# Performance work log

Measured on AMD Instinct MI355X. Metric: run time of the kernel, lower is better.

The kernel has to match this reference:

```python
import jax, jax.numpy as jnp
import numpy as np

HID = 256
NH = 8
HD = HID // NH
B = 4096
N = 64


def _xavier(key, shape):
    fan_in, fan_out = shape
    lim = float(np.sqrt(6.0 / (fan_in + fan_out)))
    return jax.random.uniform(key, shape, jnp.float32, -lim, lim)


def setup_inputs() -> dict:
    key = jax.random.key(0)
    ks = jax.random.split(key, 16)
    inp = {
        "h_recv": jax.random.normal(ks[0], (B, HID), jnp.float32),
        "h_send": jax.random.normal(ks[1], (B, N, HID), jnp.float32),
        "dist_matrix": jax.random.uniform(ks[2], (B, N), jnp.float32),
        "mask": jax.random.randint(ks[3], (B, N), 0, 2, jnp.int32),
        # projection weights stored as [in, out] (transposed vs torch Linear)
        "wq_w": _xavier(ks[4], (HID, HID)), "wq_b": jnp.zeros((HID,), jnp.float32),
        "wk_w": _xavier(ks[5], (HID, HID)), "wk_b": jnp.zeros((HID,), jnp.float32),
        "wv_w": _xavier(ks[6], (HID, HID)), "wv_b": jnp.zeros((HID,), jnp.float32),
        "d1_w": _xavier(ks[7], (HID, HID // 2)), "d1_b": jnp.zeros((HID // 2,), jnp.float32),
        "d2_w": _xavier(ks[8], (HID // 2, NH)), "d2_b": jnp.zeros((NH,), jnp.float32),
    }
    return inp


def reference(h_recv, h_send, dist_matrix, mask,
              wq_w, wq_b, wk_w, wk_b, wv_w, wv_b,
              d1_w, d1_b, d2_w, d2_b):
    b, n, hid = h_send.shape
    nh = d2_b.shape[0]
    hd = hid // nh
    # projections
    Q = (h_recv @ wq_w + wq_b).reshape(b, nh, hd)            # [B,H,D]
    K = (h_send @ wk_w + wk_b).reshape(b, n, nh, hd)          # [B,N,H,D]
    V = (h_send @ wv_w + wv_b).reshape(b, n, nh, hd)          # [B,N,H,D]
    # single-query scores per head
    scores = jnp.einsum('bhd,bnhd->bnh', Q, K) / (hd ** 0.5)  # [B,N,H]
    # MLP distance bias (softplus ensures positive slope)
    b1 = jax.nn.softplus(jax.nn.relu(h_recv @ d1_w + d1_b) @ d2_w + d2_b)  # [B,H]
    scores = scores - b1[:, None, :] * dist_matrix[:, :, None]
    # mask: zero entries -> -inf
    scores = jnp.where(mask[:, :, None] != 0, scores, -jnp.inf)
    attn = jax.nn.softmax(scores, axis=1)                     # softmax over neighbors
    z = jnp.einsum('bnh,bnhd->bhd', attn, V).reshape(b, hid)  # [B,hidden]
    return z, attn
```

## Files before the change

kernel.cpp:

```cpp
#include <hip/hip_runtime.h>
#include <math.h>

#define B_   4096
#define N_   64
#define HID_ 256
#define NH_  8
#define HD_  32
#define INV_SQRT_HD 0.17677669529663687f

typedef const float __attribute__((address_space(1)))* gbl_fp;
typedef float __attribute__((address_space(3)))* lds_fp;

__global__ __launch_bounds__(256, 2) void k1_proj(
    const float* __restrict__ h_recv,
    const float* __restrict__ wq_w, const float* __restrict__ wq_b,
    const float* __restrict__ wk_w, const float* __restrict__ wk_b,
    const float* __restrict__ d1_w, const float* __restrict__ d1_b,
    const float* __restrict__ d2_w, const float* __restrict__ d2_b,
    float* __restrict__ qh_ws, float* __restrict__ b1_ws, float* __restrict__ konst_ws)
{
    __shared__ __align__(16) float hr[8][256];
    __shared__ __align__(16) float Q[8][256];
    __shared__ float R1[8][128];
    const int t = threadIdx.x;
    const int brow = blockIdx.x * 8;

    {
        const float4* src = (const float4*)(h_recv + (size_t)brow * 256);
        float4* dst = (float4*)&hr[0][0];
        dst[t] = src[t];
        dst[t + 256] = src[t + 256];
    }
    __syncthreads();

    {
        const int j = t;
        float acc[8];
        const float bq = wq_b[j];
#pragma unroll
        for (int bb = 0; bb < 8; bb++) acc[bb] = bq;
        for (int c4 = 0; c4 < 64; c4++) {
            const float w0 = wq_w[(c4 * 4 + 0) * 256 + j];
            const float w1 = wq_w[(c4 * 4 + 1) * 256 + j];
            const float w2 = wq_w[(c4 * 4 + 2) * 256 + j];
            const float w3 = wq_w[(c4 * 4 + 3) * 256 + j];
#pragma unroll
            for (int bb = 0; bb < 8; bb++) {
                const float4 h = *(const float4*)&hr[bb][c4 * 4];
                acc[bb] += h.x * w0 + h.y * w1 + h.z * w2 + h.w * w3;
            }
        }
#pragma unroll
        for (int bb = 0; bb < 8; bb++) Q[bb][j] = acc[bb];
    }
    __syncthreads();

    {
        const int j = t & 127;
        const int bg = t >> 7;
        float acc[4];
        const float bd = d1_b[j];
#pragma unroll
        for (int r = 0; r < 4; r++) acc[r] = bd;
        for (int c4 = 0; c4 < 64; c4++) {
            const float w0 = d1_w[(c4 * 4 + 0) * 128 + j];
            const float w1 = d1_w[(c4 * 4 + 1) * 128 + j];
            const float w2 = d1_w[(c4 * 4 + 2) * 128 + j];
            const float w3 = d1_w[(c4 * 4 + 3) * 128 + j];
#pragma unroll
            for (int r = 0; r < 4; r++) {
                const float4 h = *(const float4*)&hr[bg * 4 + r][c4 * 4];
                acc[r] += h.x * w0 + h.y * w1 + h.z * w2 + h.w * w3;
            }
        }
#pragma unroll
        for (int r = 0; r < 4; r++) R1[bg * 4 + r][j] = fmaxf(acc[r], 0.0f);
    }
    __syncthreads();

    if (t < 64) {
        const int bb = t >> 3, h = t & 7;
        float acc = d2_b[h];
        for (int jj = 0; jj < 128; jj++) acc += R1[bb][jj] * d2_w[jj * 8 + h];
        const float sp = (acc > 20.0f) ? acc : log1pf(expf(acc));
        b1_ws[(size_t)(brow + bb) * 8 + h] = sp;
        float k = 0.0f;
        for (int d = 0; d < 32; d++) k += Q[bb][h * 32 + d] * wk_b[h * 32 + d];
        konst_ws[(size_t)(brow + bb) * 8 + h] = k * INV_SQRT_HD;
    }

    {
        const int c = t;
        for (int h = 0; h < 8; h++) {
            float acc[8] = {0, 0, 0, 0, 0, 0, 0, 0};
#pragma unroll
            for (int d4 = 0; d4 < 8; d4++) {
                const float4 w = *(const float4*)&wk_w[(size_t)c * 256 + h * 32 + d4 * 4];
#pragma unroll
                for (int bb = 0; bb < 8; bb++) {
                    const float4 q = *(const float4*)&Q[bb][h * 32 + d4 * 4];
                    acc[bb] += q.x * w.x + q.y * w.y + q.z * w.z + q.w * w.w;
                }
            }
#pragma unroll
            for (int bb = 0; bb < 8; bb++)
                qh_ws[((size_t)(brow + bb) * 8 + h) * 256 + c] = acc[bb];
        }
    }
}

__global__ __launch_bounds__(256, 2) void k2_attn(
    const float* __restrict__ h_send,
    const float* __restrict__ dist, const int* __restrict__ mask,
    const float* __restrict__ qh_ws, const float* __restrict__ b1_ws,
    const float* __restrict__ konst_ws,
    const float* __restrict__ wv_w, const float* __restrict__ wv_b,
    float* __restrict__ z_out,
    float* __restrict__ attn_out)
{
    __shared__ __align__(16) float hs[64][260];
    __shared__ __align__(16) float qh2[8][4][68];
    __shared__ __align__(16) float sc4[64][8];
    __shared__ float dist_l[64];
    __shared__ float b1_l[8], kon_l[8];
    __shared__ int mask_l[64];

    const int t = threadIdx.x;
    const int b = blockIdx.x;
    const int w = t >> 6;
    const int l = t & 63;

    {
        const float* src = h_send + (size_t)b * 16384;
#pragma unroll
        for (int i = 0; i < 16; i++) {
            const int row = i * 4 + w;
            __builtin_amdgcn_global_load_lds((gbl_fp)(src + row * 256 + l * 4),
                                             (lds_fp)&hs[row][0], 16, 0, 0);
        }
    }
    {
        const float4* qsrc = (const float4*)(qh_ws + (size_t)b * 2048);
#pragma unroll
        for (int k = 0; k < 2; k++) {
            const int e = t + k * 256;
            const float4 v = qsrc[e];
            const int h = e >> 6;
            const int qq = (e & 63) >> 4;
            const int pos = (e & 15) * 4;
            *(float4*)&qh2[h][qq][pos] = v;
        }
        if (t < 64) {
            dist_l[t] = dist[(size_t)b * 64 + t];
            mask_l[t] = mask[(size_t)b * 64 + t];
        } else if (t < 72) {
            b1_l[t - 64] = b1_ws[(size_t)b * 8 + (t - 64)];
            kon_l[t - 64] = konst_ws[(size_t)b * 8 + (t - 64)];
        }
    }
    __syncthreads();

    {
        const int n = w * 16 + (l & 15);
        const int cq = l >> 4;
        float p[8] = {0, 0, 0, 0, 0, 0, 0, 0};
#pragma unroll 4
        for (int c4 = 0; c4 < 16; c4++) {
            const float4 hv = *(const float4*)&hs[n][cq * 64 + c4 * 4];
#pragma unroll
            for (int h = 0; h < 8; h++) {
                const float4 qv = *(const float4*)&qh2[h][cq][c4 * 4];
                p[h] += hv.x * qv.x + hv.y * qv.y + hv.z * qv.z + hv.w * qv.w;
            }
        }
#pragma unroll
        for (int h = 0; h < 8; h++) {
            p[h] += __shfl_xor(p[h], 16, 64);
            p[h] += __shfl_xor(p[h], 32, 64);
        }
        if (cq == 0) {
            const float dv = dist_l[n];
            const int mv = mask_l[n];
#pragma unroll
            for (int h = 0; h < 8; h++) {
                const float s = p[h] * INV_SQRT_HD + kon_l[h] - b1_l[h] * dv;
                sc4[n][h] = mv ? s : -1e30f;
            }
        }
    }
    __syncthreads();

    {
        const int h = 2 * w + (l >> 5);
        const int n0 = l & 31;
        const float v0 = sc4[n0][h], v1 = sc4[n0 + 32][h];
        float m = fmaxf(v0, v1);
#pragma unroll
        for (int s = 1; s < 32; s <<= 1) m = fmaxf(m, __shfl_xor(m, s, 64));
        const float e0 = __expf(v0 - m), e1 = __expf(v1 - m);
        float sum = e0 + e1;
#pragma unroll
        for (int s = 1; s < 32; s <<= 1) sum += __shfl_xor(sum, s, 64);
        const float inv = 1.0f / sum;
        sc4[n0][h] = e0 * inv;
        sc4[n0 + 32][h] = e1 * inv;
    }
    __syncthreads();

    {
        const float* sl = &sc4[0][0];
        attn_out[(size_t)b * 512 + t] = sl[t];
        attn_out[(size_t)b * 512 + t + 256] = sl[t + 256];
    }

    float acc[8] = {0, 0, 0, 0, 0, 0, 0, 0};
    {
        const int c = t;
        for (int n = 0; n < 64; n += 2) {
            const float4 a0 = *(const float4*)&sc4[n][0];
            const float4 a1 = *(const float4*)&sc4[n][4];
            const float4 c0 = *(const float4*)&sc4[n + 1][0];
            const float4 c1 = *(const float4*)&sc4[n + 1][4];
            const float h0 = hs[n][c];
            const float h1 = hs[n + 1][c];
            acc[0] += a0.x * h0 + c0.x * h1;
            acc[1] += a0.y * h0 + c0.y * h1;
            acc[2] += a0.z * h0 + c0.z * h1;
            acc[3] += a0.w * h0 + c0.w * h1;
            acc[4] += a1.x * h0 + c1.x * h1;
            acc[5] += a1.y * h0 + c1.y * h1;
            acc[6] += a1.z * h0 + c1.z * h1;
            acc[7] += a1.w * h0 + c1.w * h1;
        }
    }
    {
        float* cl = &qh2[0][0][0];
#pragma unroll
        for (int h = 0; h < 8; h++) cl[h * 272 + t] = acc[h];
    }
    __syncthreads();

    {
        const int j = t;
        const float* cl = &qh2[0][0][0] + (j >> 5) * 272;
        float accz = wv_b[j];
        for (int c4 = 0; c4 < 64; c4++) {
            const float4 cv = *(const float4*)&cl[c4 * 4];
            accz += cv.x * wv_w[(c4 * 4 + 0) * 256 + j]
                  + cv.y * wv_w[(c4 * 4 + 1) * 256 + j]
                  + cv.z * wv_w[(c4 * 4 + 2) * 256 + j]
                  + cv.w * wv_w[(c4 * 4 + 3) * 256 + j];
        }
        z_out[(size_t)b * 256 + j] = accz;
    }
}

extern "C" void kernel_launch(void* const* d_in, const int* in_sizes, int n_in,
                              void* d_out, int out_size, void* d_ws, size_t ws_size,
                              hipStream_t stream)
{
    const float* h_recv = (const float*)d_in[0];
    const float* h_send = (const float*)d_in[1];
    const float* dist   = (const float*)d_in[2];
    const int*   mask   = (const int*)d_in[3];
    const float* wq_w = (const float*)d_in[4];
    const float* wq_b = (const float*)d_in[5];
    const float* wk_w = (const float*)d_in[6];
    const float* wk_b = (const float*)d_in[7];
    const float* wv_w = (const float*)d_in[8];
    const float* wv_b = (const float*)d_in[9];
    const float* d1_w = (const float*)d_in[10];
    const float* d1_b = (const float*)d_in[11];
    const float* d2_w = (const float*)d_in[12];
    const float* d2_b = (const float*)d_in[13];

    float* z_out = (float*)d_out;
    float* attn_out = (float*)d_out + (size_t)B_ * HID_;

    float* ws = (float*)d_ws;
    const size_t QH = (size_t)B_ * 8 * 256;
    float* qh_ws = ws;
    float* b1_ws = ws + QH;
    float* konst_ws = b1_ws + (size_t)B_ * 8;

    k1_proj<<<512, 256, 0, stream>>>(h_recv, wq_w, wq_b, wk_w, wk_b,
                                     d1_w, d1_b, d2_w, d2_b,
                                     qh_ws, b1_ws, konst_ws);
    k2_attn<<<B_, 256, 0, stream>>>(h_send, dist, mask, qh_ws, b1_ws, konst_ws,
                                    wv_w, wv_b, z_out, attn_out);
}
```

Measured before the change: 514.8 us.

## Drop LDS staging of h_send in attention kernel and halve rows per projection block

The attention kernel no longer copies each batch's 64x256 h_send tile into shared memory. It reads it straight from global memory twice, once row-wise for the scores and once column-wise for the weighted sum, and relies on L2/cache for the second pass. This frees about 66KB of LDS per block so more blocks fit per CU (launch bounds raised to 6). The projection kernel now processes 4 rows per block instead of 8 with twice as many blocks, adds unroll pragmas, and reads the weights twice as often in exchange for more parallelism.

```diff
diff --git a/kernel.cpp b/kernel.cpp
--- a/kernel.cpp
+++ b/kernel.cpp
@@ -8,10 +8,7 @@
 #define HD_  32
 #define INV_SQRT_HD 0.17677669529663687f
 
-typedef const float __attribute__((address_space(1)))* gbl_fp;
-typedef float __attribute__((address_space(3)))* lds_fp;
-
-__global__ __launch_bounds__(256, 2) void k1_proj(
+__global__ __launch_bounds__(256, 4) void k1_proj(
     const float* __restrict__ h_recv,
     const float* __restrict__ wq_w, const float* __restrict__ wq_b,
     const float* __restrict__ wk_w, const float* __restrict__ wk_b,
@@ -19,66 +16,67 @@
     const float* __restrict__ d2_w, const float* __restrict__ d2_b,
     float* __restrict__ qh_ws, float* __restrict__ b1_ws, float* __restrict__ konst_ws)
 {
-    __shared__ __align__(16) float hr[8][256];
-    __shared__ __align__(16) float Q[8][256];
-    __shared__ float R1[8][128];
+    __shared__ __align__(16) float hr[4][256];
+    __shared__ __align__(16) float Q[4][256];
+    __shared__ float R1[4][128];
     const int t = threadIdx.x;
-    const int brow = blockIdx.x * 8;
+    const int brow = blockIdx.x * 4;
 
     {
         const float4* src = (const float4*)(h_recv + (size_t)brow * 256);
         float4* dst = (float4*)&hr[0][0];
         dst[t] = src[t];
-        dst[t + 256] = src[t + 256];
     }
     __syncthreads();
 
     {
         const int j = t;
-        float acc[8];
+        float acc[4];
         const float bq = wq_b[j];
 #pragma unroll
-        for (int bb = 0; bb < 8; bb++) acc[bb] = bq;
+        for (int r = 0; r < 4; r++) acc[r] = bq;
+#pragma unroll 4
         for (int c4 = 0; c4 < 64; c4++) {
             const float w0 = wq_w[(c4 * 4 + 0) * 256 + j];
             const float w1 = wq_w[(c4 * 4 + 1) * 256 + j];
             const float w2 = wq_w[(c4 * 4 + 2) * 256 + j];
             const float w3 = wq_w[(c4 * 4 + 3) * 256 + j];
 #pragma unroll
-            for (int bb = 0; bb < 8; bb++) {
-                const float4 h = *(const float4*)&hr[bb][c4 * 4];
-                acc[bb] += h.x * w0 + h.y * w1 + h.z * w2 + h.w * w3;
-            }
-        }
-#pragma unroll
-        for (int bb = 0; bb < 8; bb++) Q[bb][j] = acc[bb];
+            for (int r = 0; r < 4; r++) {
+                const float4 h = *(const float4*)&hr[r][c4 * 4];
+                acc[r] += h.x * w0 + h.y * w1 + h.z * w2 + h.w * w3;
+            }
+        }
+#pragma unroll
+        for (int r = 0; r < 4; r++) Q[r][j] = acc[r];
     }
     __syncthreads();
 
     {
         const int j = t & 127;
         const int bg = t >> 7;
-        float acc[4];
+        float acc[2];
         const float bd = d1_b[j];
 #pragma unroll
-        for (int r = 0; r < 4; r++) acc[r] = bd;
+        for (int r = 0; r < 2; r++) acc[r] = bd;
+#pragma unroll 4
         for (int c4 = 0; c4 < 64; c4++) {
             const float w0 = d1_w[(c4 * 4 + 0) * 128 + j];
             const float w1 = d1_w[(c4 * 4 + 1) * 128 + j];
             const float w2 = d1_w[(c4 * 4 + 2) * 128 + j];
             const float w3 = d1_w[(c4 * 4 + 3) * 128 + j];
 #pragma unroll
-            for (int r = 0; r < 4; r++) {
-                const float4 h = *(const float4*)&hr[bg * 4 + r][c4 * 4];
+            for (int r = 0; r < 2; r++) {
+                const float4 h = *(const float4*)&hr[bg * 2 + r][c4 * 4];
                 acc[r] += h.x * w0 + h.y * w1 + h.z * w2 + h.w * w3;
             }
         }
 #pragma unroll
-        for (int r = 0; r < 4; r++) R1[bg * 4 + r][j] = fmaxf(acc[r], 0.0f);
-    }
-    __syncthreads();
-
-    if (t < 64) {
+        for (int r = 0; r < 2; r++) R1[bg * 2 + r][j] = fmaxf(acc[r], 0.0f);
+    }
+    __syncthreads();
+
+    if (t < 32) {
         const int bb = t >> 3, h = t & 7;
         float acc = d2_b[h];
         for (int jj = 0; jj < 128; jj++) acc += R1[bb][jj] * d2_w[jj * 8 + h];
@@ -92,24 +90,24 @@
     {
         const int c = t;
         for (int h = 0; h < 8; h++) {
-            float acc[8] = {0, 0, 0, 0, 0, 0, 0, 0};
+            float acc[4] = {0, 0, 0, 0};
 #pragma unroll
             for (int d4 = 0; d4 < 8; d4++) {
                 const float4 w = *(const float4*)&wk_w[(size_t)c * 256 + h * 32 + d4 * 4];
 #pragma unroll
-                for (int bb = 0; bb < 8; bb++) {
-                    const float4 q = *(const float4*)&Q[bb][h * 32 + d4 * 4];
-                    acc[bb] += q.x * w.x + q.y * w.y + q.z * w.z + q.w * w.w;
+                for (int r = 0; r < 4; r++) {
+                    const float4 q = *(const float4*)&Q[r][h * 32 + d4 * 4];
+                    acc[r] += q.x * w.x + q.y * w.y + q.z * w.z + q.w * w.w;
                 }
             }
 #pragma unroll
-            for (int bb = 0; bb < 8; bb++)
-                qh_ws[((size_t)(brow + bb) * 8 + h) * 256 + c] = acc[bb];
+            for (int r = 0; r < 4; r++)
+                qh_ws[((size_t)(brow + r) * 8 + h) * 256 + c] = acc[r];
         }
     }
 }
 
-__global__ __launch_bounds__(256, 2) void k2_attn(
+__global__ __launch_bounds__(256, 6) void k2_attn(
     const float* __restrict__ h_send,
     const float* __restrict__ dist, const int* __restrict__ mask,
     const float* __restrict__ qh_ws, const float* __restrict__ b1_ws,
@@ -118,7 +116,6 @@
     float* __restrict__ z_out,
     float* __restrict__ attn_out)
 {
-    __shared__ __align__(16) float hs[64][260];
     __shared__ __align__(16) float qh2[8][4][68];
     __shared__ __align__(16) float sc4[64][8];
     __shared__ float dist_l[64];
@@ -130,15 +127,6 @@
     const int w = t >> 6;
     const int l = t & 63;
 
-    {
-        const float* src = h_send + (size_t)b * 16384;
-#pragma unroll
-        for (int i = 0; i < 16; i++) {
-            const int row = i * 4 + w;
-            __builtin_amdgcn_global_load_lds((gbl_fp)(src + row * 256 + l * 4),
-                                             (lds_fp)&hs[row][0], 16, 0, 0);
-        }
-    }
     {
         const float4* qsrc = (const float4*)(qh_ws + (size_t)b * 2048);
 #pragma unroll
@@ -163,10 +151,11 @@
     {
         const int n = w * 16 + (l & 15);
         const int cq = l >> 4;
+        const float* hrow = h_send + (size_t)b * 16384 + n * 256 + cq * 64;
         float p[8] = {0, 0, 0, 0, 0, 0, 0, 0};
 #pragma unroll 4
         for (int c4 = 0; c4 < 16; c4++) {
-            const float4 hv = *(const float4*)&hs[n][cq * 64 + c4 * 4];
+            const float4 hv = *(const float4*)&hrow[c4 * 4];
 #pragma unroll
             for (int h = 0; h < 8; h++) {
                 const float4 qv = *(const float4*)&qh2[h][cq][c4 * 4];
@@ -215,14 +204,14 @@
 
     float acc[8] = {0, 0, 0, 0, 0, 0, 0, 0};
     {
-        const int c = t;
+        const float* hcol = h_send + (size_t)b * 16384 + t;
         for (int n = 0; n < 64; n += 2) {
             const float4 a0 = *(const float4*)&sc4[n][0];
             const float4 a1 = *(const float4*)&sc4[n][4];
             const float4 c0 = *(const float4*)&sc4[n + 1][0];
             const float4 c1 = *(const float4*)&sc4[n + 1][4];
-            const float h0 = hs[n][c];
-            const float h1 = hs[n + 1][c];
+            const float h0 = hcol[n * 256];
+            const float h1 = hcol[n * 256 + 256];
             acc[0] += a0.x * h0 + c0.x * h1;
             acc[1] += a0.y * h0 + c0.y * h1;
             acc[2] += a0.z * h0 + c0.z * h1;
@@ -244,6 +233,7 @@
         const int j = t;
         const float* cl = &qh2[0][0][0] + (j >> 5) * 272;
         float accz = wv_b[j];
+#pragma unroll 4
         for (int c4 = 0; c4 < 64; c4++) {
             const float4 cv = *(const float4*)&cl[c4 * 4];
             accz += cv.x * wv_w[(c4 * 4 + 0) * 256 + j]
@@ -283,9 +273,9 @@
     float* b1_ws = ws + QH;
     float* konst_ws = b1_ws + (size_t)B_ * 8;
 
-    k1_proj<<<512, 256, 0, stream>>>(h_recv, wq_w, wq_b, wk_w, wk_b,
-                                     d1_w, d1_b, d2_w, d2_b,
-                                     qh_ws, b1_ws, konst_ws);
+    k1_proj<<<1024, 256, 0, stream>>>(h_recv, wq_w, wq_b, wk_w, wk_b,
+                                      d1_w, d1_b, d2_w, d2_b,
+                                      qh_ws, b1_ws, konst_ws);
     k2_attn<<<B_, 256, 0, stream>>>(h_send, dist, mask, qh_ws, b1_ws, konst_ws,
                                     wv_w, wv_b, z_out, attn_out);
 }
```

Measured after the change: 498.2 us. 3.2% less time.
